# Kernel tuning notes

Hardware: AMD Instinct MI355X
Metric: run time of the kernel (lower is better)

## Reference

```python
import jax, jax.numpy as jnp
import numpy as np

TAU = 2.0      # LIFNode default tau
VTH = 1.0      # v_threshold
ALPHA = 2.0    # ATan surrogate alpha
EPS = 1e-5     # BatchNorm eps
SCALE = 0.125  # hardcoded attention scale
HEADS = 8

@jax.custom_vjp
def atan_spike(x):
    return (x >= 0.0).astype(x.dtype)

def _atan_fwd(x):
    return atan_spike(x), x

def _atan_bwd(x, g):
    sg = (ALPHA / 2.0) / (1.0 + (jnp.pi / 2.0 * ALPHA * x) ** 2)
    return (g * sg,)

atan_spike.defvjp(_atan_fwd, _atan_bwd)

def lif(x_seq):
    # multi-step LIF: v' = v + (x - v)/tau ; spike = H(v'-1) ; hard reset to 0 (detach_reset)
    def step(v, x):
        v = v + (x - v) / TAU
        s = atan_spike(v - VTH)
        v = v * (1.0 - jax.lax.stop_gradient(s))
        return v, s
    _, spikes = jax.lax.scan(step, jnp.zeros_like(x_seq[0]), x_seq)
    return spikes

def bn(x, gamma, beta, mean, var):
    # inference-mode BatchNorm1d over channel axis 2 of [T,B,C,N]
    inv = gamma / jnp.sqrt(var + EPS)
    return x * inv[None, None, :, None] + (beta - mean * inv)[None, None, :, None]

def setup_inputs() -> dict:
    key = jax.random.key(0)
    ks = jax.random.split(key, 24)
    T, B, C, H, W = 4, 8, 512, 32, 32
    inp = {"x": jax.random.normal(ks[0], (T, B, C, H, W), dtype=jnp.float32)}
    i = 1
    for p in ("q", "k", "v", "proj"):
        inp[p + "_w"] = jax.random.normal(ks[i], (C, C), dtype=jnp.float32) / np.sqrt(C); i += 1
        inp[p + "_gamma"] = jax.random.uniform(ks[i], (C,), minval=0.5, maxval=1.5, dtype=jnp.float32); i += 1
        inp[p + "_beta"] = 0.1 * jax.random.normal(ks[i], (C,), dtype=jnp.float32); i += 1
        inp[p + "_mean"] = 0.1 * jax.random.normal(ks[i], (C,), dtype=jnp.float32); i += 1
        inp[p + "_var"] = jax.random.uniform(ks[i], (C,), minval=0.5, maxval=1.5, dtype=jnp.float32); i += 1
    inp["proj_b"] = 0.1 * jax.random.normal(ks[i], (C,), dtype=jnp.float32)
    return inp

def reference(x, q_w, q_gamma, q_beta, q_mean, q_var,
              k_w, k_gamma, k_beta, k_mean, k_var,
              v_w, v_gamma, v_beta, v_mean, v_var,
              proj_w, proj_gamma, proj_beta, proj_mean, proj_var, proj_b):
    T, B, C, H, W = x.shape
    N = H * W
    d = C // HEADS
    s = lif(x).reshape(T, B, C, N)  # proj_lif then flatten HW

    def branch(w, g, b, m, v_):
        y = jnp.einsum('oc,tbcn->tbon', w, s)  # conv1x1 == channel GEMM
        y = lif(bn(y, g, b, m, v_))
        # [T,B,C,N] -> [T,B,h,N,d]
        return y.reshape(T, B, HEADS, d, N).transpose(0, 1, 2, 4, 3)

    q = branch(q_w, q_gamma, q_beta, q_mean, q_var)
    k = branch(k_w, k_gamma, k_beta, k_mean, k_var)
    v = branch(v_w, v_gamma, v_beta, v_mean, v_var)

    kv = jnp.einsum('tbhnd,tbhne->tbhde', k, v)          # k^T v : [T,B,h,d,d]
    att = jnp.einsum('tbhnd,tbhde->tbhne', q, kv) * SCALE  # [T,B,h,N,d]
    att = att.transpose(0, 1, 2, 4, 3).reshape(T, B, C, N)
    a = lif(att)

    y = jnp.einsum('oc,tbcn->tbon', proj_w, a) + proj_b[None, None, :, None]
    y = bn(y, proj_gamma, proj_beta, proj_mean, proj_var)
    return y.reshape(T, B, C, H, W)
```

## Files before the change

kernel.cpp:

```cpp
#include <hip/hip_runtime.h>
#include <cstdint>
#include <cstddef>

typedef unsigned short u16;
typedef __attribute__((ext_vector_type(8))) short sh8;
typedef __attribute__((ext_vector_type(8))) _Float16 hf8;
typedef __attribute__((ext_vector_type(4))) float f4;

#define MFMA16B(a, b, c) __builtin_amdgcn_mfma_f32_16x16x32_bf16((a), (b), (c), 0, 0, 0)
#define MFMA16H(a, b, c) __builtin_amdgcn_mfma_f32_16x16x32_f16((a), (b), (c), 0, 0, 0)

__device__ __forceinline__ u16 f2bf(float f) {
  union { float f; uint32_t u; } v; v.f = f;
  uint32_t u = v.u;
  uint32_t lsb = (u >> 16) & 1u;
  return (u16)((u + 0x7fffu + lsb) >> 16);
}
__device__ __forceinline__ float bf2f(u16 h) {
  union { uint32_t u; float f; } v; v.u = ((uint32_t)h) << 16;
  return v.f;
}

__device__ __forceinline__ void aload16(const void* g, void* l) {
  __builtin_amdgcn_global_load_lds(
      (const __attribute__((address_space(1))) uint32_t*)g,
      (__attribute__((address_space(3))) uint32_t*)l, 16, 0, 0);
}

__device__ __forceinline__ void pbar() {
  __builtin_amdgcn_sched_barrier(0);
  __builtin_amdgcn_s_barrier();
  __builtin_amdgcn_sched_barrier(0);
}

#define MFMA12(Af, Bf, NB)                                                    \
  {                                                                           \
    __builtin_amdgcn_s_setprio(1);                                            \
    _Pragma("unroll") for (int nf = 0; nf < 2; ++nf)                          \
      _Pragma("unroll") for (int mf = 0; mf < 6; ++mf)                        \
        acc[mf][(NB) + nf] = MFMA16H(Af[mf], Bf[nf], acc[mf][(NB) + nf]);     \
    __builtin_amdgcn_s_setprio(0);                                            \
  }

__global__ void prep_weights(const float* __restrict__ qw, const float* __restrict__ kw,
                             const float* __restrict__ vw, const float* __restrict__ pw,
                             u16* __restrict__ w2qkv, u16* __restrict__ w2p) {
  #pragma clang fp contract(off)
  int row = blockIdx.x;
  for (int c = threadIdx.x; c < 512; c += 256) {
    const float* src;
    if (row < 1536) {
      int br = row >> 9;
      src = (br == 0 ? qw : (br == 1 ? kw : vw)) + (size_t)(row & 511) * 512;
    } else {
      src = pw + (size_t)(row - 1536) * 512;
    }
    float w = src[c];
    _Float16 h0 = (_Float16)w;
    float r1 = w - (float)h0;
    _Float16 h1 = (_Float16)r1;
    union { _Float16 h; u16 u; } u0, u1;
    u0.h = h0; u1.h = h1;
    if (row < 1536) {
      w2qkv[(size_t)row * 1024 + c] = u0.u;
      w2qkv[(size_t)row * 1024 + 512 + c] = u1.u;
    } else {
      int m = row - 1536;
      w2p[(size_t)m * 512 + c] = u0.u;
      w2p[(size_t)(512 + m) * 512 + c] = u1.u;
    }
  }
}

__global__ void bn_prep(const float* __restrict__ g, const float* __restrict__ be,
                        const float* __restrict__ mu, const float* __restrict__ va,
                        float* __restrict__ inv, float* __restrict__ add) {
  #pragma clang fp contract(off)
  int i = blockIdx.x * 256 + threadIdx.x;
  if (i < 512) {
    float iv = g[i] / sqrtf(va[i] + 1e-5f);
    inv[i] = iv;
    add[i] = be[i] - mu[i] * iv;
  }
}

__global__ __launch_bounds__(256) void lif0(const float* __restrict__ x, u16* __restrict__ sT) {
  #pragma clang fp contract(off)
  __shared__ u16 st[64 * 80];
  const int tid = threadIdx.x;
  const int n0 = blockIdx.x * 64;
  const int c0 = blockIdx.y * 64;
  const int b = blockIdx.z;
  const int cl = tid >> 2;
  const int ns = (tid & 3) * 16;
  const int nr = tid >> 2;
  const int cs = (tid & 3) * 16;
  float vv[16];
#pragma unroll
  for (int i = 0; i < 16; i++) vv[i] = 0.f;
  for (int t = 0; t < 4; ++t) {
    const float* xp = x + ((size_t)((t * 8 + b) * 512 + c0 + cl)) * 1024 + n0 + ns;
#pragma unroll
    for (int q = 0; q < 4; ++q) {
      f4 xv = *(const f4*)(xp + q * 4);
#pragma unroll
      for (int j = 0; j < 4; ++j) {
        int i = q * 4 + j;
        float v2 = vv[i] + (xv[j] - vv[i]) * 0.5f;
        int spk = (v2 - 1.0f >= 0.0f);
        st[(ns + i) * 80 + cl] = spk ? (u16)0x3C00 : (u16)0;
        vv[i] = spk ? 0.0f : v2;
      }
    }
    __syncthreads();
    u16* gp = sT + ((size_t)((t * 8 + b) * 1024 + n0 + nr)) * 512 + c0 + cs;
    *(sh8*)(gp) = *(const sh8*)&st[nr * 80 + cs];
    *(sh8*)(gp + 8) = *(const sh8*)&st[nr * 80 + cs + 8];
    __syncthreads();
  }
}

__global__ __launch_bounds__(512, 2) void qkv_gemm(
    const u16* __restrict__ w2,
    const u16* __restrict__ sT,
    const float* __restrict__ inv4, const float* __restrict__ add4,
    u16* __restrict__ qs, u16* __restrict__ ks, u16* __restrict__ vs) {
  #pragma clang fp contract(off)
  __shared__ u16 lA[2][192 * 64];
  __shared__ u16 lB[3][256 * 64];
  const int tid = threadIdx.x;
  const int bid = blockIdx.x;
  const int orig = (bid & 7) * 32 + (bid >> 3);
  const int mI = orig & 7;
  const int nI = (orig >> 3) & 3;
  const int b  = orig >> 5;
  const int m0 = mI * 192;
  const int n0 = nI * 256;
  const int wid = tid >> 6, lane = tid & 63;
  const int l15 = lane & 15, l4 = lane >> 4;
  const int wm = wid >> 2, wn = wid & 3;
  const int swz = l15 & 7;
  const int srow = tid >> 3;
  const int ss = (tid & 7) ^ (srow & 7);
  int aoff[3];
#pragma unroll
  for (int c = 0; c < 3; ++c)
    aoff[c] = (m0 + c * 64 + srow) * 1024 + (ss >> 2) * 512 + (ss & 3) * 8;
  int boff[4];
#pragma unroll
  for (int c = 0; c < 4; ++c)
    boff[c] = (n0 + c * 64 + srow) * 512 + (ss >> 2) * 32 + (ss & 3) * 8;

  auto stA = [&](int ii) {
    int k0 = (ii & 15) * 32;
    u16* d = &lA[ii & 1][0];
#pragma unroll
    for (int c = 0; c < 3; ++c)
      aload16(w2 + (size_t)(aoff[c] + k0), d + c * 4096 + tid * 8);
  };
  auto stB = [&](int P) {
    int k0 = (P & 7) * 64;
    const u16* bb = sT + (size_t)(P >> 3) * 4194304 + (size_t)b * 524288;
    u16* d = &lB[P % 3][0];
#pragma unroll
    for (int c = 0; c < 4; ++c)
      aload16(bb + (size_t)(boff[c] + k0), d + c * 4096 + tid * 8);
  };

  const f4 fz = {0.f, 0.f, 0.f, 0.f};
  f4 acc[6][4];
  f4 vst[6][4];
#pragma unroll
  for (int i = 0; i < 6; i++)
#pragma unroll
    for (int j = 0; j < 4; j++) vst[i][j] = fz;

  stA(0); stB(0); stB(1);
  asm volatile("s_waitcnt vmcnt(4)" ::: "memory");
  __builtin_amdgcn_s_barrier();
  __builtin_amdgcn_sched_barrier(0);

  for (int t = 0; t < 4; ++t) {
#pragma unroll
    for (int i = 0; i < 6; i++)
#pragma unroll
      for (int j = 0; j < 4; j++) acc[i][j] = fz;

    for (int i = 0; i < 16; ++i) {
      const int ii = t * 16 + i;
      const int P = ii >> 1;
      const u16* bufA = &lA[ii & 1][0];
      const u16* bufB = &lB[P % 3][0];
      const int sb = (ii & 1) * 4;
      const bool issueB = ((ii & 1) == 0) && (P + 2 < 32);
      hf8 A0[6], Bq[2];
#pragma unroll
      for (int mf = 0; mf < 6; ++mf) {
        int r = wm * 96 + mf * 16 + l15;
        A0[mf] = *(const hf8*)&bufA[r * 64 + ((l4 ^ swz) * 8)];
      }
#pragma unroll
      for (int nf = 0; nf < 2; ++nf) {
        int r = wn * 64 + nf * 16 + l15;
        Bq[nf] = *(const hf8*)&bufB[r * 64 + (((sb + l4) ^ swz) * 8)];
      }
      if (ii < 63) stA(ii + 1);
      if (issueB) stB(P + 2);
      pbar();
      MFMA12(A0, Bq, 0);
      hf8 B1[2];
#pragma unroll
      for (int nf = 0; nf < 2; ++nf) {
        int r = wn * 64 + (2 + nf) * 16 + l15;
        B1[nf] = *(const hf8*)&bufB[r * 64 + (((sb + l4) ^ swz) * 8)];
      }
      pbar();
      MFMA12(A0, B1, 2);
      hf8 A1[6];
#pragma unroll
      for (int mf = 0; mf < 6; ++mf) {
        int r = wm * 96 + mf * 16 + l15;
        A1[mf] = *(const hf8*)&bufA[r * 64 + (((4 + l4) ^ swz) * 8)];
      }
      pbar();
      MFMA12(A1, B1, 2);
#pragma unroll
      for (int nf = 0; nf < 2; ++nf) {
        int r = wn * 64 + nf * 16 + l15;
        Bq[nf] = *(const hf8*)&bufB[r * 64 + (((sb + l4) ^ swz) * 8)];
      }
      pbar();
      MFMA12(A1, Bq, 0);
      if (((ii & 1) == 0) && issueB) {
        asm volatile("s_waitcnt vmcnt(4)" ::: "memory");
      } else {
        asm volatile("s_waitcnt vmcnt(0)" ::: "memory");
      }
      __builtin_amdgcn_s_barrier();
      __builtin_amdgcn_sched_barrier(0);
    }
#pragma unroll
    for (int mf = 0; mf < 6; ++mf) {
      int f0 = m0 + wm * 96 + mf * 16;
      int br = f0 >> 9;
      u16* dst = br == 0 ? qs : (br == 1 ? ks : vs);
      int ocb = f0 & 511;
#pragma unroll
      for (int r = 0; r < 4; ++r) {
        int oc = ocb + l4 * 4 + r;
        float iv = inv4[br * 512 + oc];
        float ad = add4[br * 512 + oc];
        size_t rowbase = ((size_t)((t * 8 + b) * 512 + oc)) * 1024 + n0;
#pragma unroll
        for (int nf = 0; nf < 4; ++nf) {
          float z = acc[mf][nf][r] * iv + ad;
          float v2 = vst[mf][nf][r];
          v2 = v2 + (z - v2) * 0.5f;
          int spk = (v2 - 1.0f >= 0.0f);
          vst[mf][nf][r] = spk ? 0.0f : v2;
          dst[rowbase + wn * 64 + nf * 16 + l15] = spk ? (u16)0x3F80 : (u16)0;
        }
      }
    }
  }
}

__global__ __launch_bounds__(256) void kv_gemm(const u16* __restrict__ ks,
                                               const u16* __restrict__ vs,
                                               float* __restrict__ kvp) {
  const int tbh = blockIdx.x;
  const int tid = threadIdx.x;
  const int wv = tid >> 6, lane = tid & 63, l15 = lane & 15, l4 = lane >> 4;
  const size_t cb = ((size_t)(tbh >> 3) * 512 + (size_t)(tbh & 7) * 64) * 1024;
  const u16* vbase = vs + cb;
  const u16* kbase = ks + cb;
  const f4 fz = {0.f, 0.f, 0.f, 0.f};
  f4 acc[4];
#pragma unroll
  for (int i = 0; i < 4; i++) acc[i] = fz;
  for (int s = 0; s < 32; ++s) {
    int kk = s * 32 + l4 * 8;
    sh8 av = *(const sh8*)(vbase + (size_t)(wv * 16 + l15) * 1024 + kk);
#pragma unroll
    for (int df = 0; df < 4; ++df) {
      sh8 bk = *(const sh8*)(kbase + (size_t)(df * 16 + l15) * 1024 + kk);
      acc[df] = MFMA16B(av, bk, acc[df]);
    }
  }
  float* out = kvp + (size_t)tbh * 4096;
#pragma unroll
  for (int df = 0; df < 4; ++df)
#pragma unroll
    for (int r = 0; r < 4; ++r)
      out[(wv * 16 + l4 * 4 + r) * 64 + df * 16 + l15] = acc[df][r];
}

__global__ __launch_bounds__(256) void att_lif(const u16* __restrict__ qs,
                                               const float* __restrict__ kvp,
                                               u16* __restrict__ aT) {
  #pragma clang fp contract(off)
  __shared__ u16 ldsb[64 * 72 * 2 + 128 * 72];
  u16* lkhi = ldsb;
  u16* lklo = ldsb + 64 * 72;
  u16* lqT = ldsb + 64 * 72 * 2;
  u16* lsp = ldsb;
  const int tid = threadIdx.x;
  const int n0 = blockIdx.x * 128;
  const int b = blockIdx.y >> 3;
  const int h = blockIdx.y & 7;
  const int wv = tid >> 6, lane = tid & 63, l15 = lane & 15, l4 = lane >> 4;
  const int e_s = tid >> 2, ds_ = (tid & 3) * 16;
  const f4 fz = {0.f, 0.f, 0.f, 0.f};
  f4 vst[4][2];
#pragma unroll
  for (int i = 0; i < 4; i++)
#pragma unroll
    for (int j = 0; j < 2; j++) vst[i][j] = fz;

  for (int t = 0; t < 4; ++t) {
    int tb = t * 8 + b;
    int tbh = tb * 8 + h;
    {
      const float* base = kvp + (size_t)tbh * 4096 + e_s * 64 + ds_;
#pragma unroll
      for (int q = 0; q < 4; ++q) {
        f4 s4 = *(const f4*)(base + q * 4);
#pragma unroll
        for (int j = 0; j < 4; ++j) {
          float sv = s4[j];
          u16 hb = f2bf(sv);
          float lof = sv - bf2f(hb);
          lkhi[e_s * 72 + ds_ + q * 4 + j] = hb;
          lklo[e_s * 72 + ds_ + q * 4 + j] = f2bf(lof);
        }
      }
    }
    {
      const u16* qb = qs + ((size_t)tb * 512 + h * 64) * 1024 + n0;
#pragma unroll
      for (int it = 0; it < 4; ++it) {
        int lin = it * 2048 + tid * 8;
        int d = lin >> 7, j0 = lin & 127;
        sh8 qv = *(const sh8*)(qb + (size_t)d * 1024 + j0);
#pragma unroll
        for (int j = 0; j < 8; ++j) lqT[(j0 + j) * 72 + d] = (u16)qv[j];
      }
    }
    __syncthreads();
    f4 acc[4][2];
#pragma unroll
    for (int i = 0; i < 4; i++)
#pragma unroll
      for (int j = 0; j < 2; j++) acc[i][j] = fz;
#pragma unroll
    for (int ksx = 0; ksx < 2; ++ksx) {
      sh8 bq[2];
#pragma unroll
      for (int nf = 0; nf < 2; ++nf)
        bq[nf] = *(const sh8*)&lqT[(wv * 32 + nf * 16 + l15) * 72 + ksx * 32 + l4 * 8];
#pragma unroll
      for (int mf = 0; mf < 4; ++mf) {
        sh8 ah = *(const sh8*)&lkhi[(mf * 16 + l15) * 72 + ksx * 32 + l4 * 8];
        sh8 al = *(const sh8*)&lklo[(mf * 16 + l15) * 72 + ksx * 32 + l4 * 8];
#pragma unroll
        for (int nf = 0; nf < 2; ++nf) {
          acc[mf][nf] = MFMA16B(ah, bq[nf], acc[mf][nf]);
          acc[mf][nf] = MFMA16B(al, bq[nf], acc[mf][nf]);
        }
      }
    }
    __syncthreads();
#pragma unroll
    for (int mf = 0; mf < 4; ++mf)
#pragma unroll
      for (int nf = 0; nf < 2; ++nf)
#pragma unroll
        for (int r = 0; r < 4; ++r) {
          float xatt = acc[mf][nf][r] * 0.125f;
          float v2 = vst[mf][nf][r];
          v2 = v2 + (xatt - v2) * 0.5f;
          int spk = (v2 - 1.0f >= 0.0f);
          vst[mf][nf][r] = spk ? 0.0f : v2;
          int e = mf * 16 + l4 * 4 + r;
          int n = wv * 32 + nf * 16 + l15;
          lsp[n * 72 + e] = spk ? (u16)0x3C00 : (u16)0;
        }
    __syncthreads();
    {
#pragma unroll
      for (int it = 0; it < 2; ++it) {
        int lin = it * 256 + tid;
        int n = lin >> 2, es = (lin & 3) * 16;
        u16* gp = aT + ((size_t)(tb * 1024 + n0 + n)) * 512 + h * 64 + es;
        *(sh8*)gp = *(const sh8*)&lsp[n * 72 + es];
        *(sh8*)(gp + 8) = *(const sh8*)&lsp[n * 72 + es + 8];
      }
    }
    __syncthreads();
  }
}

__global__ __launch_bounds__(256, 2) void proj_gemm(
    const u16* __restrict__ w2, const u16* __restrict__ aT,
    const float* __restrict__ inv4, const float* __restrict__ add4,
    const float* __restrict__ pb, float* __restrict__ out) {
  #pragma clang fp contract(off)
  __shared__ u16 lA[2 * 128 * 32];
  __shared__ u16 lB[128 * 32];
  const int tid = threadIdx.x;
  const int m0 = blockIdx.x * 128;
  const int n0 = blockIdx.y * 128;
  const int tb = blockIdx.z;
  const int lane = tid & 63, wv = tid >> 6;
  const int l15 = lane & 15, l4 = lane >> 4;
  const int wm = wv >> 1, wn = wv & 1;
  const int rA = tid >> 2;
  const int kswz = (((tid & 3) ^ ((tid >> 3) & 3)) * 8);
  const int sA = (l4 ^ ((l15 >> 1) & 3)) * 8;

  size_t aoff[4];
#pragma unroll
  for (int c = 0; c < 4; ++c) {
    int rf = c * 64 + rA;
    int sp = rf >> 7, r = rf & 127;
    aoff[c] = (size_t)(sp * 512 + m0 + r) * 512 + kswz;
  }
  size_t boff[2];
#pragma unroll
  for (int c = 0; c < 2; ++c) boff[c] = (size_t)(c * 64 + rA) * 512 + kswz;

  const f4 fz = {0.f, 0.f, 0.f, 0.f};
  f4 acc[4][4];
#pragma unroll
  for (int i = 0; i < 4; i++)
#pragma unroll
    for (int j = 0; j < 4; j++) acc[i][j] = fz;
  const u16* aTt = aT + ((size_t)tb * 1024 + n0) * 512;

  for (int k0 = 0; k0 < 512; k0 += 32) {
#pragma unroll
    for (int c = 0; c < 4; ++c)
      aload16(w2 + aoff[c] + k0, &lA[c * 2048 + tid * 8]);
#pragma unroll
    for (int c = 0; c < 2; ++c)
      aload16(aTt + boff[c] + k0, &lB[c * 2048 + tid * 8]);
    __syncthreads();
    hf8 bfr[4];
#pragma unroll
    for (int nf = 0; nf < 4; ++nf)
      bfr[nf] = *(const hf8*)&lB[(wn * 64 + nf * 16 + l15) * 32 + sA];
#pragma unroll
    for (int sp = 0; sp < 2; ++sp) {
#pragma unroll
      for (int mf = 0; mf < 4; ++mf) {
        hf8 afr = *(const hf8*)&lA[sp * 4096 + (wm * 64 + mf * 16 + l15) * 32 + sA];
#pragma unroll
        for (int nf = 0; nf < 4; ++nf) acc[mf][nf] = MFMA16H(afr, bfr[nf], acc[mf][nf]);
      }
    }
    __syncthreads();
  }
#pragma unroll
  for (int mf = 0; mf < 4; ++mf) {
#pragma unroll
    for (int r = 0; r < 4; ++r) {
      int o = m0 + wm * 64 + mf * 16 + l4 * 4 + r;
      float iv = inv4[3 * 512 + o];
      float ad = add4[3 * 512 + o];
      float bias = pb[o];
      size_t rowbase = ((size_t)(tb * 512 + o)) * 1024 + n0;
#pragma unroll
      for (int nf = 0; nf < 4; ++nf) {
        float z = (acc[mf][nf][r] + bias) * iv + ad;
        out[rowbase + wn * 64 + nf * 16 + l15] = z;
      }
    }
  }
}

extern "C" void kernel_launch(void* const* d_in, const int* in_sizes, int n_in,
                              void* d_out, int out_size, void* d_ws, size_t ws_size,
                              hipStream_t stream) {
  const float* x = (const float*)d_in[0];
  const float* qw = (const float*)d_in[1];
  const float* kw = (const float*)d_in[6];
  const float* vw = (const float*)d_in[11];
  const float* pw = (const float*)d_in[16];
  const float* pb = (const float*)d_in[21];

  char* p = (char*)d_ws;
  u16* w2qkv = (u16*)p; p += (size_t)1536 * 1024 * 2;
  u16* w2p = (u16*)p;   p += (size_t)2 * 512 * 512 * 2;
  float* inv4 = (float*)p; p += 4 * 512 * 4;
  float* add4 = (float*)p; p += 4 * 512 * 4;
  u16* sT = (u16*)p;    p += (size_t)4 * 8 * 1024 * 512 * 2;
  u16* qs = (u16*)p;    p += (size_t)4 * 8 * 512 * 1024 * 2;
  u16* ks = (u16*)p;    p += (size_t)4 * 8 * 512 * 1024 * 2;
  u16* vs = (u16*)p;    p += (size_t)4 * 8 * 512 * 1024 * 2;
  float* kvp = (float*)p; p += (size_t)256 * 4096 * 4;
  u16* aT = sT;
  float* out = (float*)d_out;

  prep_weights<<<dim3(2048), dim3(256), 0, stream>>>(qw, kw, vw, pw, w2qkv, w2p);
  for (int s = 0; s < 4; ++s) {
    const float* g  = (const float*)d_in[2 + s * 5];
    const float* be = (const float*)d_in[3 + s * 5];
    const float* mu = (const float*)d_in[4 + s * 5];
    const float* va = (const float*)d_in[5 + s * 5];
    bn_prep<<<dim3(2), dim3(256), 0, stream>>>(g, be, mu, va, inv4 + s * 512, add4 + s * 512);
  }
  lif0<<<dim3(16, 8, 8), dim3(256), 0, stream>>>(x, sT);
  qkv_gemm<<<dim3(256), dim3(512), 0, stream>>>(w2qkv, sT, inv4, add4, qs, ks, vs);
  kv_gemm<<<dim3(256), dim3(256), 0, stream>>>(ks, vs, kvp);
  att_lif<<<dim3(8, 64), dim3(256), 0, stream>>>(qs, kvp, aT);
  proj_gemm<<<dim3(4, 8, 32), dim3(256), 0, stream>>>(w2p, aT, inv4, add4, pb, out);
}
```

Baseline: 247.3 us.

## Pipeline proj GEMM with multi-buffered async LDS loads and merge BN prep launches

Rewrites proj_gemm to use 512-thread blocks with 128x256 tiles, a K=64 B tile triple-buffered in LDS and a double-buffered A tile. Global-to-LDS loads are issued ahead of the MFMA phases, following the qkv_gemm structure, and blocks are remapped to a 1D grid with XCD-aware ordering. The split-fp16 proj weights are interleaved per row. The four bn_prep launches are fused into one. It also drops a redundant Bq reload in qkv_gemm, which relies on Bq staying unchanged within an iteration.

```diff
diff --git a/kernel.cpp b/kernel.cpp
--- a/kernel.cpp
+++ b/kernel.cpp
@@ -38,6 +38,15 @@
     __builtin_amdgcn_s_setprio(1);                                            \
     _Pragma("unroll") for (int nf = 0; nf < 2; ++nf)                          \
       _Pragma("unroll") for (int mf = 0; mf < 6; ++mf)                        \
+        acc[mf][(NB) + nf] = MFMA16H(Af[mf], Bf[nf], acc[mf][(NB) + nf]);     \
+    __builtin_amdgcn_s_setprio(0);                                            \
+  }
+
+#define MFMA8(Af, Bf, NB)                                                     \
+  {                                                                           \
+    __builtin_amdgcn_s_setprio(1);                                            \
+    _Pragma("unroll") for (int nf = 0; nf < 2; ++nf)                          \
+      _Pragma("unroll") for (int mf = 0; mf < 4; ++mf)                        \
         acc[mf][(NB) + nf] = MFMA16H(Af[mf], Bf[nf], acc[mf][(NB) + nf]);     \
     __builtin_amdgcn_s_setprio(0);                                            \
   }
@@ -66,22 +75,31 @@
       w2qkv[(size_t)row * 1024 + 512 + c] = u1.u;
     } else {
       int m = row - 1536;
-      w2p[(size_t)m * 512 + c] = u0.u;
-      w2p[(size_t)(512 + m) * 512 + c] = u1.u;
-    }
-  }
-}
-
-__global__ void bn_prep(const float* __restrict__ g, const float* __restrict__ be,
-                        const float* __restrict__ mu, const float* __restrict__ va,
+      w2p[(size_t)m * 1024 + c] = u0.u;
+      w2p[(size_t)m * 1024 + 512 + c] = u1.u;
+    }
+  }
+}
+
+__global__ void bn_prep(const float* __restrict__ g0, const float* __restrict__ b0,
+                        const float* __restrict__ m0, const float* __restrict__ v0,
+                        const float* __restrict__ g1, const float* __restrict__ b1,
+                        const float* __restrict__ m1, const float* __restrict__ v1,
+                        const float* __restrict__ g2, const float* __restrict__ b2,
+                        const float* __restrict__ m2, const float* __restrict__ v2,
+                        const float* __restrict__ g3, const float* __restrict__ b3,
+                        const float* __restrict__ m3, const float* __restrict__ v3,
                         float* __restrict__ inv, float* __restrict__ add) {
   #pragma clang fp contract(off)
-  int i = blockIdx.x * 256 + threadIdx.x;
-  if (i < 512) {
-    float iv = g[i] / sqrtf(va[i] + 1e-5f);
-    inv[i] = iv;
-    add[i] = be[i] - mu[i] * iv;
-  }
+  int s = blockIdx.x >> 1;
+  int i = (blockIdx.x & 1) * 256 + threadIdx.x;
+  const float* g  = s == 0 ? g0 : s == 1 ? g1 : s == 2 ? g2 : g3;
+  const float* be = s == 0 ? b0 : s == 1 ? b1 : s == 2 ? b2 : b3;
+  const float* mu = s == 0 ? m0 : s == 1 ? m1 : s == 2 ? m2 : m3;
+  const float* va = s == 0 ? v0 : s == 1 ? v1 : s == 2 ? v2 : v3;
+  float iv = g[i] / sqrtf(va[i] + 1e-5f);
+  inv[s * 512 + i] = iv;
+  add[s * 512 + i] = be[i] - mu[i] * iv;
 }
 
 __global__ __launch_bounds__(256) void lif0(const float* __restrict__ x, u16* __restrict__ sT) {
@@ -224,12 +242,6 @@
       }
       pbar();
       MFMA12(A1, B1, 2);
-#pragma unroll
-      for (int nf = 0; nf < 2; ++nf) {
-        int r = wn * 64 + nf * 16 + l15;
-        Bq[nf] = *(const hf8*)&bufB[r * 64 + (((sb + l4) ^ swz) * 8)];
-      }
-      pbar();
       MFMA12(A1, Bq, 0);
       if (((ii & 1) == 0) && issueB) {
         asm volatile("s_waitcnt vmcnt(4)" ::: "memory");
@@ -400,34 +412,52 @@
   }
 }
 
-__global__ __launch_bounds__(256, 2) void proj_gemm(
-    const u16* __restrict__ w2, const u16* __restrict__ aT,
+__global__ __launch_bounds__(512, 2) void proj_gemm(
+    const u16* __restrict__ w2,
+    const u16* __restrict__ aT,
     const float* __restrict__ inv4, const float* __restrict__ add4,
     const float* __restrict__ pb, float* __restrict__ out) {
   #pragma clang fp contract(off)
-  __shared__ u16 lA[2 * 128 * 32];
-  __shared__ u16 lB[128 * 32];
+  __shared__ u16 lA[2][128 * 64];
+  __shared__ u16 lB[3][256 * 64];
   const int tid = threadIdx.x;
-  const int m0 = blockIdx.x * 128;
-  const int n0 = blockIdx.y * 128;
-  const int tb = blockIdx.z;
-  const int lane = tid & 63, wv = tid >> 6;
+  const int bid = blockIdx.x;
+  const int orig = (bid & 7) * 64 + (bid >> 3);
+  const int mI = orig & 3;
+  const int nI = (orig >> 2) & 3;
+  const int tb = orig >> 4;
+  const int m0 = mI * 128;
+  const int n0 = nI * 256;
+  const int wid = tid >> 6, lane = tid & 63;
   const int l15 = lane & 15, l4 = lane >> 4;
-  const int wm = wv >> 1, wn = wv & 1;
-  const int rA = tid >> 2;
-  const int kswz = (((tid & 3) ^ ((tid >> 3) & 3)) * 8);
-  const int sA = (l4 ^ ((l15 >> 1) & 3)) * 8;
-
-  size_t aoff[4];
-#pragma unroll
-  for (int c = 0; c < 4; ++c) {
-    int rf = c * 64 + rA;
-    int sp = rf >> 7, r = rf & 127;
-    aoff[c] = (size_t)(sp * 512 + m0 + r) * 512 + kswz;
-  }
-  size_t boff[2];
-#pragma unroll
-  for (int c = 0; c < 2; ++c) boff[c] = (size_t)(c * 64 + rA) * 512 + kswz;
+  const int wm = wid >> 2, wn = wid & 3;
+  const int swz = l15 & 7;
+  const int srow = tid >> 3;
+  const int ss = (tid & 7) ^ (srow & 7);
+  int aoff[2];
+#pragma unroll
+  for (int c = 0; c < 2; ++c)
+    aoff[c] = (m0 + c * 64 + srow) * 1024 + (ss >> 2) * 512 + (ss & 3) * 8;
+  int boff[4];
+#pragma unroll
+  for (int c = 0; c < 4; ++c)
+    boff[c] = (n0 + c * 64 + srow) * 512 + (ss >> 2) * 32 + (ss & 3) * 8;
+  const u16* bb = aT + (size_t)tb * 524288;
+
+  auto stA = [&](int ii) {
+    int k0 = (ii & 15) * 32;
+    u16* d = &lA[ii & 1][0];
+#pragma unroll
+    for (int c = 0; c < 2; ++c)
+      aload16(w2 + (size_t)(aoff[c] + k0), d + c * 4096 + tid * 8);
+  };
+  auto stB = [&](int P) {
+    int k0 = (P & 7) * 64;
+    u16* d = &lB[P % 3][0];
+#pragma unroll
+    for (int c = 0; c < 4; ++c)
+      aload16(bb + (size_t)(boff[c] + k0), d + c * 4096 + tid * 8);
+  };
 
   const f4 fz = {0.f, 0.f, 0.f, 0.f};
   f4 acc[4][4];
@@ -435,30 +465,57 @@
   for (int i = 0; i < 4; i++)
 #pragma unroll
     for (int j = 0; j < 4; j++) acc[i][j] = fz;
-  const u16* aTt = aT + ((size_t)tb * 1024 + n0) * 512;
-
-  for (int k0 = 0; k0 < 512; k0 += 32) {
-#pragma unroll
-    for (int c = 0; c < 4; ++c)
-      aload16(w2 + aoff[c] + k0, &lA[c * 2048 + tid * 8]);
-#pragma unroll
-    for (int c = 0; c < 2; ++c)
-      aload16(aTt + boff[c] + k0, &lB[c * 2048 + tid * 8]);
-    __syncthreads();
-    hf8 bfr[4];
-#pragma unroll
-    for (int nf = 0; nf < 4; ++nf)
-      bfr[nf] = *(const hf8*)&lB[(wn * 64 + nf * 16 + l15) * 32 + sA];
-#pragma unroll
-    for (int sp = 0; sp < 2; ++sp) {
-#pragma unroll
-      for (int mf = 0; mf < 4; ++mf) {
-        hf8 afr = *(const hf8*)&lA[sp * 4096 + (wm * 64 + mf * 16 + l15) * 32 + sA];
-#pragma unroll
-        for (int nf = 0; nf < 4; ++nf) acc[mf][nf] = MFMA16H(afr, bfr[nf], acc[mf][nf]);
-      }
-    }
-    __syncthreads();
+
+  stA(0); stB(0); stB(1);
+  asm volatile("s_waitcnt vmcnt(4)" ::: "memory");
+  __builtin_amdgcn_s_barrier();
+  __builtin_amdgcn_sched_barrier(0);
+
+  for (int ii = 0; ii < 16; ++ii) {
+    const int P = ii >> 1;
+    const u16* bufA = &lA[ii & 1][0];
+    const u16* bufB = &lB[P % 3][0];
+    const int sb = (ii & 1) * 4;
+    const bool issueB = ((ii & 1) == 0) && (P + 2 < 8);
+    hf8 A0[4], Bq[2];
+#pragma unroll
+    for (int mf = 0; mf < 4; ++mf) {
+      int r = wm * 64 + mf * 16 + l15;
+      A0[mf] = *(const hf8*)&bufA[r * 64 + ((l4 ^ swz) * 8)];
+    }
+#pragma unroll
+    for (int nf = 0; nf < 2; ++nf) {
+      int r = wn * 64 + nf * 16 + l15;
+      Bq[nf] = *(const hf8*)&bufB[r * 64 + (((sb + l4) ^ swz) * 8)];
+    }
+    if (ii < 15) stA(ii + 1);
+    if (issueB) stB(P + 2);
+    pbar();
+    MFMA8(A0, Bq, 0);
+    hf8 B1[2];
+#pragma unroll
+    for (int nf = 0; nf < 2; ++nf) {
+      int r = wn * 64 + (2 + nf) * 16 + l15;
+      B1[nf] = *(const hf8*)&bufB[r * 64 + (((sb + l4) ^ swz) * 8)];
+    }
+    pbar();
+    MFMA8(A0, B1, 2);
+    hf8 A1[4];
+#pragma unroll
+    for (int mf = 0; mf < 4; ++mf) {
+      int r = wm * 64 + mf * 16 + l15;
+      A1[mf] = *(const hf8*)&bufA[r * 64 + (((4 + l4) ^ swz) * 8)];
+    }
+    pbar();
+    MFMA8(A1, B1, 2);
+    MFMA8(A1, Bq, 0);
+    if (((ii & 1) == 0) && issueB) {
+      asm volatile("s_waitcnt vmcnt(4)" ::: "memory");
+    } else {
+      asm volatile("s_waitcnt vmcnt(0)" ::: "memory");
+    }
+    __builtin_amdgcn_s_barrier();
+    __builtin_amdgcn_sched_barrier(0);
   }
 #pragma unroll
   for (int mf = 0; mf < 4; ++mf) {
@@ -490,7 +547,7 @@
 
   char* p = (char*)d_ws;
   u16* w2qkv = (u16*)p; p += (size_t)1536 * 1024 * 2;
-  u16* w2p = (u16*)p;   p += (size_t)2 * 512 * 512 * 2;
+  u16* w2p = (u16*)p;   p += (size_t)512 * 1024 * 2;
   float* inv4 = (float*)p; p += 4 * 512 * 4;
   float* add4 = (float*)p; p += 4 * 512 * 4;
   u16* sT = (u16*)p;    p += (size_t)4 * 8 * 1024 * 512 * 2;
@@ -502,16 +559,15 @@
   float* out = (float*)d_out;
 
   prep_weights<<<dim3(2048), dim3(256), 0, stream>>>(qw, kw, vw, pw, w2qkv, w2p);
-  for (int s = 0; s < 4; ++s) {
-    const float* g  = (const float*)d_in[2 + s * 5];
-    const float* be = (const float*)d_in[3 + s * 5];
-    const float* mu = (const float*)d_in[4 + s * 5];
-    const float* va = (const float*)d_in[5 + s * 5];
-    bn_prep<<<dim3(2), dim3(256), 0, stream>>>(g, be, mu, va, inv4 + s * 512, add4 + s * 512);
-  }
+  bn_prep<<<dim3(8), dim3(256), 0, stream>>>(
+      (const float*)d_in[2], (const float*)d_in[3], (const float*)d_in[4], (const float*)d_in[5],
+      (const float*)d_in[7], (const float*)d_in[8], (const float*)d_in[9], (const float*)d_in[10],
+      (const float*)d_in[12], (const float*)d_in[13], (const float*)d_in[14], (const float*)d_in[15],
+      (const float*)d_in[17], (const float*)d_in[18], (const float*)d_in[19], (const float*)d_in[20],
+      inv4, add4);
   lif0<<<dim3(16, 8, 8), dim3(256), 0, stream>>>(x, sT);
   qkv_gemm<<<dim3(256), dim3(512), 0, stream>>>(w2qkv, sT, inv4, add4, qs, ks, vs);
   kv_gemm<<<dim3(256), dim3(256), 0, stream>>>(ks, vs, kvp);
   att_lif<<<dim3(8, 64), dim3(256), 0, stream>>>(qs, kvp, aT);
-  proj_gemm<<<dim3(4, 8, 32), dim3(256), 0, stream>>>(w2p, aT, inv4, add4, pb, out);
-}
+  proj_gemm<<<dim3(512), dim3(512), 0, stream>>>(w2p, aT, inv4, add4, pb, out);
+}
```

New measurement: 248.1 us. Within noise of the previous version (+0.3%).

## Halve qkv GEMM M-tile, double grid, and register double-buffer LDS fragments

Applied to the files above, without the earlier changes.

The QKV GEMM block tile drops from 192 to 96 output channels, so the grid grows from 256 to 512 blocks and accumulator registers are halved. The inner loop no longer uses four barriers per k-step; it processes two k-steps per iteration and reads the next step's LDS fragments into a second register set while MFMAs run on the current one. The four separate bn_prep launches are merged into one. The smaller tile reloads the B operand from global memory twice as often, and the new barrier and waitcnt schedule risks LDS hazards if its accounting is wrong.

```diff
diff --git a/kernel.cpp b/kernel.cpp
--- a/kernel.cpp
+++ b/kernel.cpp
@@ -26,21 +26,6 @@
       (const __attribute__((address_space(1))) uint32_t*)g,
       (__attribute__((address_space(3))) uint32_t*)l, 16, 0, 0);
 }
-
-__device__ __forceinline__ void pbar() {
-  __builtin_amdgcn_sched_barrier(0);
-  __builtin_amdgcn_s_barrier();
-  __builtin_amdgcn_sched_barrier(0);
-}
-
-#define MFMA12(Af, Bf, NB)                                                    \
-  {                                                                           \
-    __builtin_amdgcn_s_setprio(1);                                            \
-    _Pragma("unroll") for (int nf = 0; nf < 2; ++nf)                          \
-      _Pragma("unroll") for (int mf = 0; mf < 6; ++mf)                        \
-        acc[mf][(NB) + nf] = MFMA16H(Af[mf], Bf[nf], acc[mf][(NB) + nf]);     \
-    __builtin_amdgcn_s_setprio(0);                                            \
-  }
 
 __global__ void prep_weights(const float* __restrict__ qw, const float* __restrict__ kw,
                              const float* __restrict__ vw, const float* __restrict__ pw,
@@ -72,16 +57,25 @@
   }
 }
 
-__global__ void bn_prep(const float* __restrict__ g, const float* __restrict__ be,
-                        const float* __restrict__ mu, const float* __restrict__ va,
+__global__ void bn_prep(const float* __restrict__ g0, const float* __restrict__ b0,
+                        const float* __restrict__ m0, const float* __restrict__ v0,
+                        const float* __restrict__ g1, const float* __restrict__ b1,
+                        const float* __restrict__ m1, const float* __restrict__ v1,
+                        const float* __restrict__ g2, const float* __restrict__ b2,
+                        const float* __restrict__ m2, const float* __restrict__ v2,
+                        const float* __restrict__ g3, const float* __restrict__ b3,
+                        const float* __restrict__ m3, const float* __restrict__ v3,
                         float* __restrict__ inv, float* __restrict__ add) {
   #pragma clang fp contract(off)
-  int i = blockIdx.x * 256 + threadIdx.x;
-  if (i < 512) {
-    float iv = g[i] / sqrtf(va[i] + 1e-5f);
-    inv[i] = iv;
-    add[i] = be[i] - mu[i] * iv;
-  }
+  int s = blockIdx.x >> 1;
+  int i = (blockIdx.x & 1) * 256 + threadIdx.x;
+  const float* g  = s == 0 ? g0 : s == 1 ? g1 : s == 2 ? g2 : g3;
+  const float* be = s == 0 ? b0 : s == 1 ? b1 : s == 2 ? b2 : b3;
+  const float* mu = s == 0 ? m0 : s == 1 ? m1 : s == 2 ? m2 : m3;
+  const float* va = s == 0 ? v0 : s == 1 ? v1 : s == 2 ? v2 : v3;
+  float iv = g[i] / sqrtf(va[i] + 1e-5f);
+  inv[s * 512 + i] = iv;
+  add[s * 512 + i] = be[i] - mu[i] * iv;
 }
 
 __global__ __launch_bounds__(256) void lif0(const float* __restrict__ x, u16* __restrict__ sT) {
@@ -126,37 +120,33 @@
     const float* __restrict__ inv4, const float* __restrict__ add4,
     u16* __restrict__ qs, u16* __restrict__ ks, u16* __restrict__ vs) {
   #pragma clang fp contract(off)
-  __shared__ u16 lA[2][192 * 64];
+  __shared__ u16 lA[2][96 * 64];
   __shared__ u16 lB[3][256 * 64];
   const int tid = threadIdx.x;
   const int bid = blockIdx.x;
-  const int orig = (bid & 7) * 32 + (bid >> 3);
-  const int mI = orig & 7;
-  const int nI = (orig >> 3) & 3;
-  const int b  = orig >> 5;
-  const int m0 = mI * 192;
+  const int orig = (bid & 7) * 64 + (bid >> 3);
+  const int mI = orig & 15;
+  const int nI = (orig >> 4) & 3;
+  const int b  = orig >> 6;
+  const int m0 = mI * 96;
   const int n0 = nI * 256;
   const int wid = tid >> 6, lane = tid & 63;
   const int l15 = lane & 15, l4 = lane >> 4;
   const int wm = wid >> 2, wn = wid & 3;
   const int swz = l15 & 7;
-  const int srow = tid >> 3;
-  const int ss = (tid & 7) ^ (srow & 7);
-  int aoff[3];
-#pragma unroll
-  for (int c = 0; c < 3; ++c)
-    aoff[c] = (m0 + c * 64 + srow) * 1024 + (ss >> 2) * 512 + (ss & 3) * 8;
+  const int ss = (tid & 7) ^ ((tid >> 3) & 7);
+  const int aoff1 = (m0 + (tid >> 3)) * 1024 + (ss >> 2) * 512 + (ss & 3) * 8;
+  const int aoff2 = aoff1 + 64 * 1024;
   int boff[4];
 #pragma unroll
   for (int c = 0; c < 4; ++c)
-    boff[c] = (n0 + c * 64 + srow) * 512 + (ss >> 2) * 32 + (ss & 3) * 8;
-
-  auto stA = [&](int ii) {
-    int k0 = (ii & 15) * 32;
-    u16* d = &lA[ii & 1][0];
-#pragma unroll
-    for (int c = 0; c < 3; ++c)
-      aload16(w2 + (size_t)(aoff[c] + k0), d + c * 4096 + tid * 8);
+    boff[c] = (n0 + c * 64 + (tid >> 3)) * 512 + (ss >> 2) * 32 + (ss & 3) * 8;
+
+  auto stA = [&](int j) {
+    int k0 = (j & 15) * 32;
+    u16* d = &lA[j & 1][0];
+    aload16(w2 + (size_t)(aoff1 + k0), d + tid * 8);
+    if (tid < 256) aload16(w2 + (size_t)(aoff2 + k0), d + 4096 + tid * 8);
   };
   auto stB = [&](int P) {
     int k0 = (P & 7) * 64;
@@ -168,80 +158,81 @@
   };
 
   const f4 fz = {0.f, 0.f, 0.f, 0.f};
-  f4 acc[6][4];
-  f4 vst[6][4];
-#pragma unroll
-  for (int i = 0; i < 6; i++)
+  f4 acc[3][4];
+  f4 vst[3][4];
+#pragma unroll
+  for (int i = 0; i < 3; i++)
 #pragma unroll
     for (int j = 0; j < 4; j++) vst[i][j] = fz;
 
-  stA(0); stB(0); stB(1);
+  hf8 Ae0[3], Ae1[3], Be[4];
+  hf8 Ao0[3], Ao1[3], Bo[4];
+
+#define READF(A0_, A1_, B_, jj)                                               \
+  {                                                                           \
+    const u16* bA = &lA[(jj) & 1][0];                                         \
+    const u16* bB = &lB[((jj) >> 1) % 3][0];                                  \
+    const int sb_ = ((jj) & 1) * 4;                                           \
+    _Pragma("unroll") for (int mf = 0; mf < 3; ++mf) {                        \
+      int r_ = wm * 48 + mf * 16 + l15;                                       \
+      A0_[mf] = *(const hf8*)&bA[r_ * 64 + ((l4 ^ swz) * 8)];                 \
+      A1_[mf] = *(const hf8*)&bA[r_ * 64 + (((4 + l4) ^ swz) * 8)];           \
+    }                                                                         \
+    _Pragma("unroll") for (int nf = 0; nf < 4; ++nf) {                        \
+      int r_ = wn * 64 + nf * 16 + l15;                                       \
+      B_[nf] = *(const hf8*)&bB[r_ * 64 + (((sb_ + l4) ^ swz) * 8)];          \
+    }                                                                         \
+  }
+
+#define TILE_MFMA(A0_, A1_, B_)                                               \
+  {                                                                           \
+    __builtin_amdgcn_s_setprio(1);                                            \
+    _Pragma("unroll") for (int nf = 0; nf < 4; ++nf)                          \
+      _Pragma("unroll") for (int mf = 0; mf < 3; ++mf)                        \
+        acc[mf][nf] = MFMA16H(A0_[mf], B_[nf], acc[mf][nf]);                  \
+    _Pragma("unroll") for (int nf = 0; nf < 4; ++nf)                          \
+      _Pragma("unroll") for (int mf = 0; mf < 3; ++mf)                        \
+        acc[mf][nf] = MFMA16H(A1_[mf], B_[nf], acc[mf][nf]);                  \
+    __builtin_amdgcn_s_setprio(0);                                            \
+  }
+
+  stA(0); stA(1); stB(0); stB(1);
   asm volatile("s_waitcnt vmcnt(4)" ::: "memory");
   __builtin_amdgcn_s_barrier();
   __builtin_amdgcn_sched_barrier(0);
+  READF(Ae0, Ae1, Be, 0);
 
   for (int t = 0; t < 4; ++t) {
 #pragma unroll
-    for (int i = 0; i < 6; i++)
+    for (int i = 0; i < 3; i++)
 #pragma unroll
       for (int j = 0; j < 4; j++) acc[i][j] = fz;
 
-    for (int i = 0; i < 16; ++i) {
-      const int ii = t * 16 + i;
+    for (int p = 0; p < 8; ++p) {
+      const int ii = t * 16 + p * 2;
       const int P = ii >> 1;
-      const u16* bufA = &lA[ii & 1][0];
-      const u16* bufB = &lB[P % 3][0];
-      const int sb = (ii & 1) * 4;
-      const bool issueB = ((ii & 1) == 0) && (P + 2 < 32);
-      hf8 A0[6], Bq[2];
-#pragma unroll
-      for (int mf = 0; mf < 6; ++mf) {
-        int r = wm * 96 + mf * 16 + l15;
-        A0[mf] = *(const hf8*)&bufA[r * 64 + ((l4 ^ swz) * 8)];
-      }
-#pragma unroll
-      for (int nf = 0; nf < 2; ++nf) {
-        int r = wn * 64 + nf * 16 + l15;
-        Bq[nf] = *(const hf8*)&bufB[r * 64 + (((sb + l4) ^ swz) * 8)];
-      }
-      if (ii < 63) stA(ii + 1);
+      stA(ii + 2);
+      const bool issueB = (P + 2 < 32);
       if (issueB) stB(P + 2);
-      pbar();
-      MFMA12(A0, Bq, 0);
-      hf8 B1[2];
-#pragma unroll
-      for (int nf = 0; nf < 2; ++nf) {
-        int r = wn * 64 + (2 + nf) * 16 + l15;
-        B1[nf] = *(const hf8*)&bufB[r * 64 + (((sb + l4) ^ swz) * 8)];
-      }
-      pbar();
-      MFMA12(A0, B1, 2);
-      hf8 A1[6];
-#pragma unroll
-      for (int mf = 0; mf < 6; ++mf) {
-        int r = wm * 96 + mf * 16 + l15;
-        A1[mf] = *(const hf8*)&bufA[r * 64 + (((4 + l4) ^ swz) * 8)];
-      }
-      pbar();
-      MFMA12(A1, B1, 2);
-#pragma unroll
-      for (int nf = 0; nf < 2; ++nf) {
-        int r = wn * 64 + nf * 16 + l15;
-        Bq[nf] = *(const hf8*)&bufB[r * 64 + (((sb + l4) ^ swz) * 8)];
-      }
-      pbar();
-      MFMA12(A1, Bq, 0);
-      if (((ii & 1) == 0) && issueB) {
+      READF(Ao0, Ao1, Bo, ii + 1);
+      TILE_MFMA(Ae0, Ae1, Be);
+      if (issueB) {
         asm volatile("s_waitcnt vmcnt(4)" ::: "memory");
       } else {
         asm volatile("s_waitcnt vmcnt(0)" ::: "memory");
       }
       __builtin_amdgcn_s_barrier();
       __builtin_amdgcn_sched_barrier(0);
-    }
-#pragma unroll
-    for (int mf = 0; mf < 6; ++mf) {
-      int f0 = m0 + wm * 96 + mf * 16;
+      stA(ii + 3);
+      READF(Ae0, Ae1, Be, ii + 2);
+      TILE_MFMA(Ao0, Ao1, Bo);
+      asm volatile("s_waitcnt vmcnt(0)" ::: "memory");
+      __builtin_amdgcn_s_barrier();
+      __builtin_amdgcn_sched_barrier(0);
+    }
+#pragma unroll
+    for (int mf = 0; mf < 3; ++mf) {
+      int f0 = m0 + wm * 48 + mf * 16;
       int br = f0 >> 9;
       u16* dst = br == 0 ? qs : (br == 1 ? ks : vs);
       int ocb = f0 & 511;
@@ -263,6 +254,8 @@
       }
     }
   }
+#undef READF
+#undef TILE_MFMA
 }
 
 __global__ __launch_bounds__(256) void kv_gemm(const u16* __restrict__ ks,
@@ -502,15 +495,14 @@
   float* out = (float*)d_out;
 
   prep_weights<<<dim3(2048), dim3(256), 0, stream>>>(qw, kw, vw, pw, w2qkv, w2p);
-  for (int s = 0; s < 4; ++s) {
-    const float* g  = (const float*)d_in[2 + s * 5];
-    const float* be = (const float*)d_in[3 + s * 5];
-    const float* mu = (const float*)d_in[4 + s * 5];
-    const float* va = (const float*)d_in[5 + s * 5];
-    bn_prep<<<dim3(2), dim3(256), 0, stream>>>(g, be, mu, va, inv4 + s * 512, add4 + s * 512);
-  }
+  bn_prep<<<dim3(8), dim3(256), 0, stream>>>(
+      (const float*)d_in[2], (const float*)d_in[3], (const float*)d_in[4], (const float*)d_in[5],
+      (const float*)d_in[7], (const float*)d_in[8], (const float*)d_in[9], (const float*)d_in[10],
+      (const float*)d_in[12], (const float*)d_in[13], (const float*)d_in[14], (const float*)d_in[15],
+      (const float*)d_in[17], (const float*)d_in[18], (const float*)d_in[19], (const float*)d_in[20],
+      inv4, add4);
   lif0<<<dim3(16, 8, 8), dim3(256), 0, stream>>>(x, sT);
-  qkv_gemm<<<dim3(256), dim3(512), 0, stream>>>(w2qkv, sT, inv4, add4, qs, ks, vs);
+  qkv_gemm<<<dim3(512), dim3(512), 0, stream>>>(w2qkv, sT, inv4, add4, qs, ks, vs);
   kv_gemm<<<dim3(256), dim3(256), 0, stream>>>(ks, vs, kvp);
   att_lif<<<dim3(8, 64), dim3(256), 0, stream>>>(qs, kvp, aT);
   proj_gemm<<<dim3(4, 8, 32), dim3(256), 0, stream>>>(w2p, aT, inv4, add4, pb, out);
```

New measurement: 306.6 us. +24.0%, slower.

## Store K/V spikes as int8 and compute k^T v with int8 MFMA

Applied to the files above, without the earlier changes.

The qkv GEMM epilogue now writes K and V spikes as one-byte 0/1 values instead of bf16, and kv_gemm reads them and accumulates with the i32 16x16x64 int8 MFMA, converting the integer counts to float at the end. This halves the K/V write and read traffic and halves the MFMA iteration count in kv_gemm, and the result stays exact because spikes are binary. Separately, the four bn_prep launches are merged into one 8-block launch to cut launch overhead. The epilogue now branches per branch type, which may add a little divergence to the stores.

```diff
diff --git a/kernel.cpp b/kernel.cpp
--- a/kernel.cpp
+++ b/kernel.cpp
@@ -3,12 +3,15 @@
 #include <cstddef>
 
 typedef unsigned short u16;
+typedef unsigned char u8;
 typedef __attribute__((ext_vector_type(8))) short sh8;
 typedef __attribute__((ext_vector_type(8))) _Float16 hf8;
 typedef __attribute__((ext_vector_type(4))) float f4;
+typedef __attribute__((ext_vector_type(4))) int i4;
 
 #define MFMA16B(a, b, c) __builtin_amdgcn_mfma_f32_16x16x32_bf16((a), (b), (c), 0, 0, 0)
 #define MFMA16H(a, b, c) __builtin_amdgcn_mfma_f32_16x16x32_f16((a), (b), (c), 0, 0, 0)
+#define MFMAI8(a, b, c)  __builtin_amdgcn_mfma_i32_16x16x64_i8((a), (b), (c), 0, 0, 0)
 
 __device__ __forceinline__ u16 f2bf(float f) {
   union { float f; uint32_t u; } v; v.f = f;
@@ -25,12 +28,6 @@
   __builtin_amdgcn_global_load_lds(
       (const __attribute__((address_space(1))) uint32_t*)g,
       (__attribute__((address_space(3))) uint32_t*)l, 16, 0, 0);
-}
-
-__device__ __forceinline__ void pbar() {
-  __builtin_amdgcn_sched_barrier(0);
-  __builtin_amdgcn_s_barrier();
-  __builtin_amdgcn_sched_barrier(0);
 }
 
 #define MFMA12(Af, Bf, NB)                                                    \
@@ -72,16 +69,25 @@
   }
 }
 
-__global__ void bn_prep(const float* __restrict__ g, const float* __restrict__ be,
-                        const float* __restrict__ mu, const float* __restrict__ va,
+__global__ void bn_prep(const float* __restrict__ g0, const float* __restrict__ b0,
+                        const float* __restrict__ m0, const float* __restrict__ v0,
+                        const float* __restrict__ g1, const float* __restrict__ b1,
+                        const float* __restrict__ m1, const float* __restrict__ v1,
+                        const float* __restrict__ g2, const float* __restrict__ b2,
+                        const float* __restrict__ m2, const float* __restrict__ v2,
+                        const float* __restrict__ g3, const float* __restrict__ b3,
+                        const float* __restrict__ m3, const float* __restrict__ v3,
                         float* __restrict__ inv, float* __restrict__ add) {
   #pragma clang fp contract(off)
-  int i = blockIdx.x * 256 + threadIdx.x;
-  if (i < 512) {
-    float iv = g[i] / sqrtf(va[i] + 1e-5f);
-    inv[i] = iv;
-    add[i] = be[i] - mu[i] * iv;
-  }
+  int s = blockIdx.x >> 1;
+  int i = (blockIdx.x & 1) * 256 + threadIdx.x;
+  const float* g  = s == 0 ? g0 : s == 1 ? g1 : s == 2 ? g2 : g3;
+  const float* be = s == 0 ? b0 : s == 1 ? b1 : s == 2 ? b2 : b3;
+  const float* mu = s == 0 ? m0 : s == 1 ? m1 : s == 2 ? m2 : m3;
+  const float* va = s == 0 ? v0 : s == 1 ? v1 : s == 2 ? v2 : v3;
+  float iv = g[i] / sqrtf(va[i] + 1e-5f);
+  inv[s * 512 + i] = iv;
+  add[s * 512 + i] = be[i] - mu[i] * iv;
 }
 
 __global__ __launch_bounds__(256) void lif0(const float* __restrict__ x, u16* __restrict__ sT) {
@@ -124,7 +130,7 @@
     const u16* __restrict__ w2,
     const u16* __restrict__ sT,
     const float* __restrict__ inv4, const float* __restrict__ add4,
-    u16* __restrict__ qs, u16* __restrict__ ks, u16* __restrict__ vs) {
+    u16* __restrict__ qs, u8* __restrict__ ks8, u8* __restrict__ vs8) {
   #pragma clang fp contract(off)
   __shared__ u16 lA[2][192 * 64];
   __shared__ u16 lB[3][256 * 64];
@@ -206,7 +212,9 @@
       }
       if (ii < 63) stA(ii + 1);
       if (issueB) stB(P + 2);
-      pbar();
+      __builtin_amdgcn_sched_barrier(0);
+      __builtin_amdgcn_s_barrier();
+      __builtin_amdgcn_sched_barrier(0);
       MFMA12(A0, Bq, 0);
       hf8 B1[2];
 #pragma unroll
@@ -214,7 +222,9 @@
         int r = wn * 64 + (2 + nf) * 16 + l15;
         B1[nf] = *(const hf8*)&bufB[r * 64 + (((sb + l4) ^ swz) * 8)];
       }
-      pbar();
+      __builtin_amdgcn_sched_barrier(0);
+      __builtin_amdgcn_s_barrier();
+      __builtin_amdgcn_sched_barrier(0);
       MFMA12(A0, B1, 2);
       hf8 A1[6];
 #pragma unroll
@@ -222,14 +232,18 @@
         int r = wm * 96 + mf * 16 + l15;
         A1[mf] = *(const hf8*)&bufA[r * 64 + (((4 + l4) ^ swz) * 8)];
       }
-      pbar();
+      __builtin_amdgcn_sched_barrier(0);
+      __builtin_amdgcn_s_barrier();
+      __builtin_amdgcn_sched_barrier(0);
       MFMA12(A1, B1, 2);
 #pragma unroll
       for (int nf = 0; nf < 2; ++nf) {
         int r = wn * 64 + nf * 16 + l15;
         Bq[nf] = *(const hf8*)&bufB[r * 64 + (((sb + l4) ^ swz) * 8)];
       }
-      pbar();
+      __builtin_amdgcn_sched_barrier(0);
+      __builtin_amdgcn_s_barrier();
+      __builtin_amdgcn_sched_barrier(0);
       MFMA12(A1, Bq, 0);
       if (((ii & 1) == 0) && issueB) {
         asm volatile("s_waitcnt vmcnt(4)" ::: "memory");
@@ -243,7 +257,6 @@
     for (int mf = 0; mf < 6; ++mf) {
       int f0 = m0 + wm * 96 + mf * 16;
       int br = f0 >> 9;
-      u16* dst = br == 0 ? qs : (br == 1 ? ks : vs);
       int ocb = f0 & 511;
 #pragma unroll
       for (int r = 0; r < 4; ++r) {
@@ -258,33 +271,39 @@
           v2 = v2 + (z - v2) * 0.5f;
           int spk = (v2 - 1.0f >= 0.0f);
           vst[mf][nf][r] = spk ? 0.0f : v2;
-          dst[rowbase + wn * 64 + nf * 16 + l15] = spk ? (u16)0x3F80 : (u16)0;
+          size_t idx = rowbase + wn * 64 + nf * 16 + l15;
+          if (br == 0) {
+            qs[idx] = spk ? (u16)0x3F80 : (u16)0;
+          } else {
+            u8* d8 = (br == 1) ? ks8 : vs8;
+            d8[idx] = (u8)spk;
+          }
         }
       }
     }
   }
 }
 
-__global__ __launch_bounds__(256) void kv_gemm(const u16* __restrict__ ks,
-                                               const u16* __restrict__ vs,
+__global__ __launch_bounds__(256) void kv_gemm(const u8* __restrict__ ks8,
+                                               const u8* __restrict__ vs8,
                                                float* __restrict__ kvp) {
   const int tbh = blockIdx.x;
   const int tid = threadIdx.x;
   const int wv = tid >> 6, lane = tid & 63, l15 = lane & 15, l4 = lane >> 4;
   const size_t cb = ((size_t)(tbh >> 3) * 512 + (size_t)(tbh & 7) * 64) * 1024;
-  const u16* vbase = vs + cb;
-  const u16* kbase = ks + cb;
-  const f4 fz = {0.f, 0.f, 0.f, 0.f};
-  f4 acc[4];
-#pragma unroll
-  for (int i = 0; i < 4; i++) acc[i] = fz;
-  for (int s = 0; s < 32; ++s) {
-    int kk = s * 32 + l4 * 8;
-    sh8 av = *(const sh8*)(vbase + (size_t)(wv * 16 + l15) * 1024 + kk);
+  const u8* vbase = vs8 + cb;
+  const u8* kbase = ks8 + cb;
+  const i4 iz = {0, 0, 0, 0};
+  i4 acc[4];
+#pragma unroll
+  for (int i = 0; i < 4; i++) acc[i] = iz;
+  for (int s = 0; s < 16; ++s) {
+    int kk = s * 64 + l4 * 16;
+    i4 av = *(const i4*)(vbase + (size_t)(wv * 16 + l15) * 1024 + kk);
 #pragma unroll
     for (int df = 0; df < 4; ++df) {
-      sh8 bk = *(const sh8*)(kbase + (size_t)(df * 16 + l15) * 1024 + kk);
-      acc[df] = MFMA16B(av, bk, acc[df]);
+      i4 bk = *(const i4*)(kbase + (size_t)(df * 16 + l15) * 1024 + kk);
+      acc[df] = MFMAI8(av, bk, acc[df]);
     }
   }
   float* out = kvp + (size_t)tbh * 4096;
@@ -292,7 +311,7 @@
   for (int df = 0; df < 4; ++df)
 #pragma unroll
     for (int r = 0; r < 4; ++r)
-      out[(wv * 16 + l4 * 4 + r) * 64 + df * 16 + l15] = acc[df][r];
+      out[(wv * 16 + l4 * 4 + r) * 64 + df * 16 + l15] = (float)acc[df][r];
 }
 
 __global__ __launch_bounds__(256) void att_lif(const u16* __restrict__ qs,
@@ -495,23 +514,22 @@
   float* add4 = (float*)p; p += 4 * 512 * 4;
   u16* sT = (u16*)p;    p += (size_t)4 * 8 * 1024 * 512 * 2;
   u16* qs = (u16*)p;    p += (size_t)4 * 8 * 512 * 1024 * 2;
-  u16* ks = (u16*)p;    p += (size_t)4 * 8 * 512 * 1024 * 2;
-  u16* vs = (u16*)p;    p += (size_t)4 * 8 * 512 * 1024 * 2;
+  u8* ks8 = (u8*)p;     p += (size_t)4 * 8 * 512 * 1024;
+  u8* vs8 = (u8*)p;     p += (size_t)4 * 8 * 512 * 1024;
   float* kvp = (float*)p; p += (size_t)256 * 4096 * 4;
   u16* aT = sT;
   float* out = (float*)d_out;
 
   prep_weights<<<dim3(2048), dim3(256), 0, stream>>>(qw, kw, vw, pw, w2qkv, w2p);
-  for (int s = 0; s < 4; ++s) {
-    const float* g  = (const float*)d_in[2 + s * 5];
-    const float* be = (const float*)d_in[3 + s * 5];
-    const float* mu = (const float*)d_in[4 + s * 5];
-    const float* va = (const float*)d_in[5 + s * 5];
-    bn_prep<<<dim3(2), dim3(256), 0, stream>>>(g, be, mu, va, inv4 + s * 512, add4 + s * 512);
-  }
+  bn_prep<<<dim3(8), dim3(256), 0, stream>>>(
+      (const float*)d_in[2], (const float*)d_in[3], (const float*)d_in[4], (const float*)d_in[5],
+      (const float*)d_in[7], (const float*)d_in[8], (const float*)d_in[9], (const float*)d_in[10],
+      (const float*)d_in[12], (const float*)d_in[13], (const float*)d_in[14], (const float*)d_in[15],
+      (const float*)d_in[17], (const float*)d_in[18], (const float*)d_in[19], (const float*)d_in[20],
+      inv4, add4);
   lif0<<<dim3(16, 8, 8), dim3(256), 0, stream>>>(x, sT);
-  qkv_gemm<<<dim3(256), dim3(512), 0, stream>>>(w2qkv, sT, inv4, add4, qs, ks, vs);
-  kv_gemm<<<dim3(256), dim3(256), 0, stream>>>(ks, vs, kvp);
+  qkv_gemm<<<dim3(256), dim3(512), 0, stream>>>(w2qkv, sT, inv4, add4, qs, ks8, vs8);
+  kv_gemm<<<dim3(256), dim3(256), 0, stream>>>(ks8, vs8, kvp);
   att_lif<<<dim3(8, 64), dim3(256), 0, stream>>>(qs, kvp, aT);
   proj_gemm<<<dim3(4, 8, 32), dim3(256), 0, stream>>>(w2p, aT, inv4, add4, pb, out);
 }
```

Measured after the change: 277.3 us. +12.1%, slower.
